# Optimization experiments

Measured on AMD Instinct MI355X. Metric: run time of the kernel, lower is better.

The kernel has to match this reference:

```python
import jax, jax.numpy as jnp
import numpy as np

EPS = 1e-5
QB = 127.0  # int8 activation quantization bound

def rmsnorm(x):
    # SimpleRMSNorm: x / rms(x), no learned scale
    return x * jax.lax.rsqrt(jnp.mean(x * x, axis=-1, keepdims=True) + EPS)

def activation_quant(x):
    # per-token absmax int8 quant-dequant
    scale = QB / jnp.clip(jnp.max(jnp.abs(x), axis=-1, keepdims=True), EPS)
    return jnp.clip(jnp.round(x * scale), -QB - 1, QB) / scale

def weight_quant(w):
    # per-tensor ternary quant-dequant (BitNet b1.58)
    scale = 1.0 / jnp.clip(jnp.mean(jnp.abs(w)), EPS)
    return jnp.clip(jnp.round(w * scale), -1.0, 1.0) / scale

def ste(x, q):
    # straight-through estimator: forward uses q, gradient flows to x
    return x + jax.lax.stop_gradient(q - x)

def bitlinear(x, w, b):
    xn = rmsnorm(x)
    xq = ste(xn, activation_quant(xn))
    wq = ste(w, weight_quant(w))
    # x: [b, s, d_in], w: [d_out, d_in] -> [b, s, d_out]
    return jnp.einsum('bsd,od->bso', xq, wq) + b

def setup_inputs() -> dict:
    key = jax.random.key(0)
    k1, k2, k3, k4, k5 = jax.random.split(key, 5)
    dim, inner = 1024, 4096
    x = jax.random.normal(k1, (4, 4096, dim), dtype=jnp.float32)
    w1 = jax.random.normal(k2, (inner, dim), dtype=jnp.float32) * (dim ** -0.5)
    b1 = jax.random.normal(k3, (inner,), dtype=jnp.float32) * 0.02
    w2 = jax.random.normal(k4, (dim, inner), dtype=jnp.float32) * (inner ** -0.5)
    b2 = jax.random.normal(k5, (dim,), dtype=jnp.float32) * 0.02
    return {"x": x, "w1": w1, "b1": b1, "w2": w2, "b2": b2}

def reference(x, w1, b1, w2, b2):
    h = jax.nn.gelu(bitlinear(x, w1, b1), approximate=False)  # torch nn.GELU default = exact erf
    # dropout p=0.0 is identity; post_act_ln disabled
    return bitlinear(h, w2, b2)
```

## Files before the change

### kernel.cpp

```cpp
#include <hip/hip_runtime.h>

#define TOK   16384
#define DIM   1024
#define INNER 4096
#define EPSF  1e-5f

typedef int v4i  __attribute__((ext_vector_type(4)));
typedef int v16i __attribute__((ext_vector_type(16)));

static __device__ __forceinline__ void async_copy16(const char* g, char* l) {
    __builtin_amdgcn_global_load_lds(
        (const __attribute__((address_space(1))) unsigned int*)g,
        (__attribute__((address_space(3))) unsigned int*)l, 16, 0, 0);
}

static __device__ __forceinline__ float bf2f(unsigned short u) {
    return __uint_as_float(((unsigned)u) << 16);
}
static __device__ __forceinline__ unsigned short f2bf(float f) {
    unsigned u = __float_as_uint(f);
    return (unsigned short)((u + 0x7fffu + ((u >> 16) & 1u)) >> 16);
}

static __device__ __forceinline__ float fast_erf(float z) {
    float az = fabsf(z);
    float tt = __builtin_amdgcn_rcpf(1.f + 0.3275911f * az);
    float poly = ((((1.061405429f * tt - 1.453152027f) * tt + 1.421413741f) * tt
                   - 0.284496736f) * tt + 0.254829592f) * tt;
    float er = 1.f - poly * __expf(-az * az);
    return copysignf(er, z);
}
static __device__ __forceinline__ float gelu_exact(float v) {
    return 0.5f * v * (1.f + fast_erf(v * 0.70710678118654752f));
}

static __device__ __forceinline__ float waveSum(float v) {
#pragma unroll
    for (int o = 32; o > 0; o >>= 1) v += __shfl_down(v, o, 64);
    return v;
}
static __device__ __forceinline__ float waveMax(float v) {
#pragma unroll
    for (int o = 32; o > 0; o >>= 1) v = fmaxf(v, __shfl_down(v, o, 64));
    return v;
}

__global__ void absmean_k(const float* __restrict__ w, int n4, float* __restrict__ acc) {
    int idx = blockIdx.x * blockDim.x + threadIdx.x;
    int stride = gridDim.x * blockDim.x;
    const float4* w4 = (const float4*)w;
    float s = 0.f;
    for (int i = idx; i < n4; i += stride) {
        float4 v = w4[i];
        s += fabsf(v.x) + fabsf(v.y) + fabsf(v.z) + fabsf(v.w);
    }
    __shared__ float sp[4];
    int wv = threadIdx.x >> 6, lane = threadIdx.x & 63;
    s = waveSum(s);
    if (lane == 0) sp[wv] = s;
    __syncthreads();
    if (threadIdx.x == 0) atomicAdd(acc, sp[0] + sp[1] + sp[2] + sp[3]);
}

__global__ void wquant_k(const float* __restrict__ w, int n,
                         const float* __restrict__ acc, float* __restrict__ wscale,
                         char* __restrict__ wq) {
    float mean = *acc / (float)n;
    float cl = fmaxf(mean, EPSF);
    float s = 1.f / cl;
    if (blockIdx.x == 0 && threadIdx.x == 0) *wscale = cl;
    int idx = blockIdx.x * blockDim.x + threadIdx.x;
    int stride = gridDim.x * blockDim.x;
    int n4 = n >> 2;
    const float4* w4 = (const float4*)w;
    unsigned* q4 = (unsigned*)wq;
    for (int i = idx; i < n4; i += stride) {
        float4 v = w4[i];
        float e[4] = {v.x, v.y, v.z, v.w};
        unsigned packed = 0;
#pragma unroll
        for (int j = 0; j < 4; j++) {
            float r = rintf(e[j] * s);
            r = fminf(fmaxf(r, -1.f), 1.f);
            packed |= ((unsigned)((int)r & 0xff)) << (8 * j);
        }
        q4[i] = packed;
    }
}

template <int D, int VPT>
__global__ void actquant_f32_k(const float* __restrict__ X, char* __restrict__ Q,
                               float* __restrict__ rs_out) {
    int token = blockIdx.x;
    int t = threadIdx.x;
    const float4* xp = (const float4*)(X + (long)token * D);
    float vals[VPT];
    float ss = 0.f, am = 0.f;
#pragma unroll
    for (int j = 0; j < VPT / 4; j++) {
        float4 v = xp[t * (VPT / 4) + j];
        vals[4 * j] = v.x; vals[4 * j + 1] = v.y; vals[4 * j + 2] = v.z; vals[4 * j + 3] = v.w;
        ss += v.x * v.x + v.y * v.y + v.z * v.z + v.w * v.w;
        am = fmaxf(am, fmaxf(fmaxf(fabsf(v.x), fabsf(v.y)), fmaxf(fabsf(v.z), fabsf(v.w))));
    }
    __shared__ float sp[8];
    __shared__ float bc[2];
    int wv = t >> 6, lane = t & 63;
    float S = waveSum(ss);
    float M = waveMax(am);
    if (lane == 0) { sp[wv] = S; sp[4 + wv] = M; }
    __syncthreads();
    if (t == 0) {
        float Sa = sp[0] + sp[1] + sp[2] + sp[3];
        float Ma = fmaxf(fmaxf(sp[4], sp[5]), fmaxf(sp[6], sp[7]));
        float rinv = rsqrtf(Sa * (1.f / (float)D) + EPSF);
        float amn = Ma * rinv;
        float scale = 127.f / fmaxf(amn, EPSF);
        rs_out[token] = 1.f / scale;
        bc[0] = rinv; bc[1] = scale;
    }
    __syncthreads();
    float rinv = bc[0], scale = bc[1];
    unsigned outw[VPT / 4];
#pragma unroll
    for (int j = 0; j < VPT; j++) {
        float r = rintf((vals[j] * rinv) * scale);
        r = fminf(fmaxf(r, -128.f), 127.f);
        unsigned qi = (unsigned)((int)r & 0xff) << (8 * (j & 3));
        if ((j & 3) == 0) outw[j / 4] = qi; else outw[j / 4] |= qi;
    }
    unsigned* qp = (unsigned*)(Q + (long)token * D);
#pragma unroll
    for (int j = 0; j < VPT / 4; j++) qp[t * (VPT / 4) + j] = outw[j];
}

template <int D, int VPT>
__global__ void actquant_bf16_k(const unsigned short* __restrict__ X, char* __restrict__ Q,
                                float* __restrict__ rs_out) {
    int token = blockIdx.x;
    int t = threadIdx.x;
    const uint4* xp = (const uint4*)(X + (long)token * D);
    float vals[VPT];
    float ss = 0.f, am = 0.f;
#pragma unroll
    for (int j = 0; j < VPT / 8; j++) {
        uint4 v = xp[t * (VPT / 8) + j];
        unsigned ws[4] = {v.x, v.y, v.z, v.w};
#pragma unroll
        for (int p = 0; p < 4; p++) {
            float f0 = gelu_exact(bf2f((unsigned short)(ws[p] & 0xffff)));
            float f1 = gelu_exact(bf2f((unsigned short)(ws[p] >> 16)));
            vals[8 * j + 2 * p] = f0; vals[8 * j + 2 * p + 1] = f1;
            ss += f0 * f0 + f1 * f1;
            am = fmaxf(am, fmaxf(fabsf(f0), fabsf(f1)));
        }
    }
    __shared__ float sp[8];
    __shared__ float bc[2];
    int wv = t >> 6, lane = t & 63;
    float S = waveSum(ss);
    float M = waveMax(am);
    if (lane == 0) { sp[wv] = S; sp[4 + wv] = M; }
    __syncthreads();
    if (t == 0) {
        float Sa = sp[0] + sp[1] + sp[2] + sp[3];
        float Ma = fmaxf(fmaxf(sp[4], sp[5]), fmaxf(sp[6], sp[7]));
        float rinv = rsqrtf(Sa * (1.f / (float)D) + EPSF);
        float amn = Ma * rinv;
        float scale = 127.f / fmaxf(amn, EPSF);
        rs_out[token] = 1.f / scale;
        bc[0] = rinv; bc[1] = scale;
    }
    __syncthreads();
    float rinv = bc[0], scale = bc[1];
    unsigned outw[4];
#pragma unroll
    for (int j = 0; j < VPT; j++) {
        float r = rintf((vals[j] * rinv) * scale);
        r = fminf(fmaxf(r, -128.f), 127.f);
        unsigned qi = (unsigned)((int)r & 0xff) << (8 * (j & 3));
        if ((j & 3) == 0) outw[j / 4] = qi; else outw[j / 4] |= qi;
    }
    uint4* qp = (uint4*)(Q + (long)token * D);
    qp[t] = make_uint4(outw[0], outw[1], outw[2], outw[3]);
}

template <int OUT_F32>
__global__ __launch_bounds__(512, 2) void gemm8_k(
    const char* __restrict__ A, const char* __restrict__ Bw,
    const float* __restrict__ rs, const float* __restrict__ wscale_p,
    const float* __restrict__ bias, void* __restrict__ outp,
    int M, int N, int K) {
    __shared__ char L[131072];
    int t = threadIdx.x;
    int lane = t & 63, wv = t >> 6;
    int l31 = lane & 31, kh = lane >> 5;
    int wmi = wv >> 2, wni = wv & 3;
    int m0 = blockIdx.y * 256, n0 = blockIdx.x * 256;

    int srow = t >> 3;
    int scol = ((t & 7) ^ (srow & 7)) * 16;
    const char* srcA = A + (long)(m0 + srow) * K + scol;
    const char* srcB = Bw + (long)(n0 + srow) * K + scol;
    char* ldsA = L + (size_t)t * 16;
    char* ldsB = L + 65536 + (size_t)t * 16;
    long k64 = (long)64 * K;

    auto stA = [&](int Tt, int half) {
        const char* g = srcA + (long)(half * 128) * K + (long)Tt * 128;
        char* l = ldsA + (Tt & 1) * 32768 + half * 16384;
        async_copy16(g, l);
        async_copy16(g + k64, l + 8192);
    };
    auto stB = [&](int Tt, int half) {
        const char* g = srcB + (long)(half * 128) * K + (long)Tt * 128;
        char* l = ldsB + (Tt & 1) * 32768 + half * 16384;
        async_copy16(g, l);
        async_copy16(g + k64, l + 8192);
    };

    int slot[4];
#pragma unroll
    for (int ks = 0; ks < 4; ks++) slot[ks] = ((2 * ks + kh) ^ (l31 & 7)) * 16;
    int rowA[2][2], rowB[2];
#pragma unroll
    for (int ih = 0; ih < 2; ih++)
#pragma unroll
        for (int il = 0; il < 2; il++)
            rowA[ih][il] = (ih * 128 + il * 64 + wmi * 32 + l31) * 128;
#pragma unroll
    for (int jh = 0; jh < 2; jh++) rowB[jh] = 65536 + (jh * 128 + wni * 32 + l31) * 128;

    v16i acc[4][2] = {};
    int nK = K >> 7;

    stA(0, 0); stA(0, 1); stB(0, 0); stB(0, 1);
    stB(1, 0); stA(1, 1);
    asm volatile("s_waitcnt vmcnt(4)" ::: "memory");
    asm volatile("s_barrier" ::: "memory");

#pragma unroll 2
    for (int T = 0; T < nK; ++T) {
        int bo = (T & 1) * 32768;
        v4i a[2][4], bb[4];
#pragma unroll
        for (int il = 0; il < 2; il++)
#pragma unroll
            for (int ks = 0; ks < 4; ks++)
                a[il][ks] = *(const v4i*)(L + bo + rowA[0][il] + slot[ks]);
#pragma unroll
        for (int ks = 0; ks < 4; ks++)
            bb[ks] = *(const v4i*)(L + bo + rowB[0] + slot[ks]);
        if (T + 1 < nK) stA(T + 1, 0);
        asm volatile("s_barrier" ::: "memory");
        __builtin_amdgcn_s_setprio(1);
#pragma unroll
        for (int ks = 0; ks < 4; ks++) {
            acc[0][0] = __builtin_amdgcn_mfma_i32_32x32x32_i8(a[0][ks], bb[ks], acc[0][0], 0, 0, 0);
            acc[1][0] = __builtin_amdgcn_mfma_i32_32x32x32_i8(a[1][ks], bb[ks], acc[1][0], 0, 0, 0);
        }
        __builtin_amdgcn_s_setprio(0);
        asm volatile("s_barrier" ::: "memory");
#pragma unroll
        for (int il = 0; il < 2; il++)
#pragma unroll
            for (int ks = 0; ks < 4; ks++)
                a[il][ks] = *(const v4i*)(L + bo + rowA[1][il] + slot[ks]);
        if (T + 1 < nK) stB(T + 1, 1);
        asm volatile("s_barrier" ::: "memory");
        __builtin_amdgcn_s_setprio(1);
#pragma unroll
        for (int ks = 0; ks < 4; ks++) {
            acc[2][0] = __builtin_amdgcn_mfma_i32_32x32x32_i8(a[0][ks], bb[ks], acc[2][0], 0, 0, 0);
            acc[3][0] = __builtin_amdgcn_mfma_i32_32x32x32_i8(a[1][ks], bb[ks], acc[3][0], 0, 0, 0);
        }
        __builtin_amdgcn_s_setprio(0);
        asm volatile("s_barrier" ::: "memory");
#pragma unroll
        for (int ks = 0; ks < 4; ks++)
            bb[ks] = *(const v4i*)(L + bo + rowB[1] + slot[ks]);
        if (T + 2 < nK) stB(T + 2, 0);
        asm volatile("s_barrier" ::: "memory");
        __builtin_amdgcn_s_setprio(1);
#pragma unroll
        for (int ks = 0; ks < 4; ks++) {
            acc[2][1] = __builtin_amdgcn_mfma_i32_32x32x32_i8(a[0][ks], bb[ks], acc[2][1], 0, 0, 0);
            acc[3][1] = __builtin_amdgcn_mfma_i32_32x32x32_i8(a[1][ks], bb[ks], acc[3][1], 0, 0, 0);
        }
        __builtin_amdgcn_s_setprio(0);
        asm volatile("s_barrier" ::: "memory");
#pragma unroll
        for (int il = 0; il < 2; il++)
#pragma unroll
            for (int ks = 0; ks < 4; ks++)
                a[il][ks] = *(const v4i*)(L + bo + rowA[0][il] + slot[ks]);
        if (T + 2 < nK) stA(T + 2, 1);
        asm volatile("s_barrier" ::: "memory");
        __builtin_amdgcn_s_setprio(1);
#pragma unroll
        for (int ks = 0; ks < 4; ks++) {
            acc[0][1] = __builtin_amdgcn_mfma_i32_32x32x32_i8(a[0][ks], bb[ks], acc[0][1], 0, 0, 0);
            acc[1][1] = __builtin_amdgcn_mfma_i32_32x32x32_i8(a[1][ks], bb[ks], acc[1][1], 0, 0, 0);
        }
        __builtin_amdgcn_s_setprio(0);
        asm volatile("s_waitcnt vmcnt(4)" ::: "memory");
        asm volatile("s_barrier" ::: "memory");
    }

    float wsc = *wscale_p;
    float bv[2];
#pragma unroll
    for (int j = 0; j < 2; j++) bv[j] = bias[n0 + j * 128 + wni * 32 + l31];
#pragma unroll
    for (int i = 0; i < 4; i++) {
        int mbase = m0 + i * 64 + wmi * 32 + 4 * kh;
        float fsv[16];
#pragma unroll
        for (int rg = 0; rg < 16; rg++)
            fsv[rg] = rs[mbase + (rg & 3) + 8 * (rg >> 2)] * wsc;
#pragma unroll
        for (int j = 0; j < 2; j++) {
            int ng = n0 + j * 128 + wni * 32 + l31;
#pragma unroll
            for (int rg = 0; rg < 16; rg++) {
                int mg = mbase + (rg & 3) + 8 * (rg >> 2);
                float v = (float)acc[i][j][rg] * fsv[rg] + bv[j];
                long idx = (long)mg * N + ng;
                if (OUT_F32) ((float*)outp)[idx] = v;
                else ((unsigned short*)outp)[idx] = f2bf(v);
            }
        }
    }
}

extern "C" void kernel_launch(void* const* d_in, const int* in_sizes, int n_in,
                              void* d_out, int out_size, void* d_ws, size_t ws_size,
                              hipStream_t stream) {
    const float* x  = (const float*)d_in[0];
    const float* w1 = (const float*)d_in[1];
    const float* b1 = (const float*)d_in[2];
    const float* w2 = (const float*)d_in[3];
    const float* b2 = (const float*)d_in[4];
    float* out = (float*)d_out;

    char* ws = (char*)d_ws;
    float* acc1 = (float*)(ws + 0);
    float* acc2 = (float*)(ws + 4);
    float* wsc1 = (float*)(ws + 8);
    float* wsc2 = (float*)(ws + 12);
    size_t off = 256;
    char* w1q = ws + off; off += (size_t)INNER * DIM;
    char* w2q = ws + off; off += (size_t)INNER * DIM;
    char* xq1 = ws + off; off += (size_t)TOK * DIM;
    float* rs1 = (float*)(ws + off); off += (size_t)TOK * 4;
    char* xq2 = ws + off; off += (size_t)TOK * INNER;
    float* rs2 = (float*)(ws + off); off += (size_t)TOK * 4;
    unsigned short* h = (unsigned short*)(ws + off);

    hipMemsetAsync(d_ws, 0, 16, stream);

    int nw = INNER * DIM;
    absmean_k<<<1024, 256, 0, stream>>>(w1, nw / 4, acc1);
    absmean_k<<<1024, 256, 0, stream>>>(w2, nw / 4, acc2);
    wquant_k<<<2048, 256, 0, stream>>>(w1, nw, acc1, wsc1, w1q);
    wquant_k<<<2048, 256, 0, stream>>>(w2, nw, acc2, wsc2, w2q);

    actquant_f32_k<DIM, 4><<<TOK, 256, 0, stream>>>(x, xq1, rs1);
    gemm8_k<0><<<dim3(INNER / 256, TOK / 256), 512, 0, stream>>>(
        xq1, w1q, rs1, wsc1, b1, (void*)h, TOK, INNER, DIM);
    actquant_bf16_k<INNER, 16><<<TOK, 256, 0, stream>>>(h, xq2, rs2);
    gemm8_k<1><<<dim3(DIM / 256, TOK / 256), 512, 0, stream>>>(
        xq2, w2q, rs2, wsc2, b2, (void*)out, TOK, DIM, INNER);
}
```

Baseline: 391.4 us.

## Restructure int8 GEMM LDS layout to k-major slabs with per-kstep pipelining

Replaces the row-major XOR-swizzled LDS tile layout with a k-block-major layout where each 16-byte k-chunk of all 256 rows is stored contiguously, and reassigns warps to contiguous 128x64 output subtiles. The main loop now issues one k-step of 8 MFMAs per barrier pair, interleaving the four async stage-loads for the next tile across k-steps with a single-tile lookahead instead of the previous two-stage staggered schedule. This aims for conflict-free LDS reads without swizzle and better MFMA density per barrier, at the cost of losing deeper prefetch and changing global load coalescing, since each thread now reads 16 bytes per row at stride K.

Result: slower. 439.2 us (+12.2%).

```diff
diff --git a/kernel.cpp b/kernel.cpp
--- a/kernel.cpp
+++ b/kernel.cpp
@@ -198,129 +198,87 @@
     int wmi = wv >> 2, wni = wv & 3;
     int m0 = blockIdx.y * 256, n0 = blockIdx.x * 256;
 
-    int srow = t >> 3;
-    int scol = ((t & 7) ^ (srow & 7)) * 16;
-    const char* srcA = A + (long)(m0 + srow) * K + scol;
-    const char* srcB = Bw + (long)(n0 + srow) * K + scol;
-    char* ldsA = L + (size_t)t * 16;
-    char* ldsB = L + 65536 + (size_t)t * 16;
-    long k64 = (long)64 * K;
-
-    auto stA = [&](int Tt, int half) {
-        const char* g = srcA + (long)(half * 128) * K + (long)Tt * 128;
-        char* l = ldsA + (Tt & 1) * 32768 + half * 16384;
+    const char* srcA0 = A  + (long)(m0 + (t & 255)) * K + ((t >> 8) * 16);
+    const char* srcB0 = Bw + (long)(n0 + (t & 255)) * K + ((t >> 8) * 16);
+    char* dA = L + (size_t)t * 16;
+    char* dB = L + 32768 + (size_t)t * 16;
+
+    auto stA = [&](int Tt, int kb) {
+        const char* g = srcA0 + ((long)Tt << 7) + kb * 64;
+        char* l = dA + (Tt & 1) * 65536 + kb * 16384;
         async_copy16(g, l);
-        async_copy16(g + k64, l + 8192);
+        async_copy16(g + 32, l + 8192);
     };
-    auto stB = [&](int Tt, int half) {
-        const char* g = srcB + (long)(half * 128) * K + (long)Tt * 128;
-        char* l = ldsB + (Tt & 1) * 32768 + half * 16384;
+    auto stB = [&](int Tt, int kb) {
+        const char* g = srcB0 + ((long)Tt << 7) + kb * 64;
+        char* l = dB + (Tt & 1) * 65536 + kb * 16384;
         async_copy16(g, l);
-        async_copy16(g + k64, l + 8192);
+        async_copy16(g + 32, l + 8192);
     };
 
-    int slot[4];
-#pragma unroll
-    for (int ks = 0; ks < 4; ks++) slot[ks] = ((2 * ks + kh) ^ (l31 & 7)) * 16;
-    int rowA[2][2], rowB[2];
-#pragma unroll
-    for (int ih = 0; ih < 2; ih++)
-#pragma unroll
-        for (int il = 0; il < 2; il++)
-            rowA[ih][il] = (ih * 128 + il * 64 + wmi * 32 + l31) * 128;
-#pragma unroll
-    for (int jh = 0; jh < 2; jh++) rowB[jh] = 65536 + (jh * 128 + wni * 32 + l31) * 128;
+    const char* rdA = L + kh * 4096 + (size_t)(wmi * 128 + l31) * 16;
+    const char* rdB = L + 32768 + kh * 4096 + (size_t)(wni * 64 + l31) * 16;
 
     v16i acc[4][2] = {};
     int nK = K >> 7;
 
-    stA(0, 0); stA(0, 1); stB(0, 0); stB(0, 1);
-    stB(1, 0); stA(1, 1);
+    stA(0, 0); stB(0, 0); stA(0, 1); stB(0, 1);
     asm volatile("s_waitcnt vmcnt(4)" ::: "memory");
-    asm volatile("s_barrier" ::: "memory");
-
-#pragma unroll 2
+    __builtin_amdgcn_s_barrier();
+
     for (int T = 0; T < nK; ++T) {
-        int bo = (T & 1) * 32768;
-        v4i a[2][4], bb[4];
-#pragma unroll
-        for (int il = 0; il < 2; il++)
-#pragma unroll
-            for (int ks = 0; ks < 4; ks++)
-                a[il][ks] = *(const v4i*)(L + bo + rowA[0][il] + slot[ks]);
-#pragma unroll
-        for (int ks = 0; ks < 4; ks++)
-            bb[ks] = *(const v4i*)(L + bo + rowB[0] + slot[ks]);
-        if (T + 1 < nK) stA(T + 1, 0);
-        asm volatile("s_barrier" ::: "memory");
-        __builtin_amdgcn_s_setprio(1);
-#pragma unroll
-        for (int ks = 0; ks < 4; ks++) {
-            acc[0][0] = __builtin_amdgcn_mfma_i32_32x32x32_i8(a[0][ks], bb[ks], acc[0][0], 0, 0, 0);
-            acc[1][0] = __builtin_amdgcn_mfma_i32_32x32x32_i8(a[1][ks], bb[ks], acc[1][0], 0, 0, 0);
+        int bo = (T & 1) * 65536;
+        bool pre = (T + 1 < nK);
+#pragma unroll
+        for (int ks = 0; ks < 4; ++ks) {
+            const char* pa = rdA + bo + ks * 8192;
+            const char* pb = rdB + bo + ks * 8192;
+            v4i a0 = *(const v4i*)(pa);
+            v4i a1 = *(const v4i*)(pa + 512);
+            v4i a2 = *(const v4i*)(pa + 1024);
+            v4i a3 = *(const v4i*)(pa + 1536);
+            v4i b0 = *(const v4i*)(pb);
+            v4i b1 = *(const v4i*)(pb + 512);
+            if (pre) {
+                if (ks == 0) stA(T + 1, 0);
+                else if (ks == 1) stB(T + 1, 0);
+                else if (ks == 2) stA(T + 1, 1);
+                else stB(T + 1, 1);
+            }
+            __builtin_amdgcn_s_barrier();
+            __builtin_amdgcn_s_setprio(1);
+            acc[0][0] = __builtin_amdgcn_mfma_i32_32x32x32_i8(a0, b0, acc[0][0], 0, 0, 0);
+            acc[0][1] = __builtin_amdgcn_mfma_i32_32x32x32_i8(a0, b1, acc[0][1], 0, 0, 0);
+            acc[1][0] = __builtin_amdgcn_mfma_i32_32x32x32_i8(a1, b0, acc[1][0], 0, 0, 0);
+            acc[1][1] = __builtin_amdgcn_mfma_i32_32x32x32_i8(a1, b1, acc[1][1], 0, 0, 0);
+            acc[2][0] = __builtin_amdgcn_mfma_i32_32x32x32_i8(a2, b0, acc[2][0], 0, 0, 0);
+            acc[2][1] = __builtin_amdgcn_mfma_i32_32x32x32_i8(a2, b1, acc[2][1], 0, 0, 0);
+            acc[3][0] = __builtin_amdgcn_mfma_i32_32x32x32_i8(a3, b0, acc[3][0], 0, 0, 0);
+            acc[3][1] = __builtin_amdgcn_mfma_i32_32x32x32_i8(a3, b1, acc[3][1], 0, 0, 0);
+            __builtin_amdgcn_s_setprio(0);
+            if (ks == 1) {
+                if (pre) asm volatile("s_waitcnt vmcnt(4)" ::: "memory");
+                else     asm volatile("s_waitcnt vmcnt(0)" ::: "memory");
+            }
+            if (ks == 3 && pre) asm volatile("s_waitcnt vmcnt(4)" ::: "memory");
+            __builtin_amdgcn_s_barrier();
         }
-        __builtin_amdgcn_s_setprio(0);
-        asm volatile("s_barrier" ::: "memory");
-#pragma unroll
-        for (int il = 0; il < 2; il++)
-#pragma unroll
-            for (int ks = 0; ks < 4; ks++)
-                a[il][ks] = *(const v4i*)(L + bo + rowA[1][il] + slot[ks]);
-        if (T + 1 < nK) stB(T + 1, 1);
-        asm volatile("s_barrier" ::: "memory");
-        __builtin_amdgcn_s_setprio(1);
-#pragma unroll
-        for (int ks = 0; ks < 4; ks++) {
-            acc[2][0] = __builtin_amdgcn_mfma_i32_32x32x32_i8(a[0][ks], bb[ks], acc[2][0], 0, 0, 0);
-            acc[3][0] = __builtin_amdgcn_mfma_i32_32x32x32_i8(a[1][ks], bb[ks], acc[3][0], 0, 0, 0);
-        }
-        __builtin_amdgcn_s_setprio(0);
-        asm volatile("s_barrier" ::: "memory");
-#pragma unroll
-        for (int ks = 0; ks < 4; ks++)
-            bb[ks] = *(const v4i*)(L + bo + rowB[1] + slot[ks]);
-        if (T + 2 < nK) stB(T + 2, 0);
-        asm volatile("s_barrier" ::: "memory");
-        __builtin_amdgcn_s_setprio(1);
-#pragma unroll
-        for (int ks = 0; ks < 4; ks++) {
-            acc[2][1] = __builtin_amdgcn_mfma_i32_32x32x32_i8(a[0][ks], bb[ks], acc[2][1], 0, 0, 0);
-            acc[3][1] = __builtin_amdgcn_mfma_i32_32x32x32_i8(a[1][ks], bb[ks], acc[3][1], 0, 0, 0);
-        }
-        __builtin_amdgcn_s_setprio(0);
-        asm volatile("s_barrier" ::: "memory");
-#pragma unroll
-        for (int il = 0; il < 2; il++)
-#pragma unroll
-            for (int ks = 0; ks < 4; ks++)
-                a[il][ks] = *(const v4i*)(L + bo + rowA[0][il] + slot[ks]);
-        if (T + 2 < nK) stA(T + 2, 1);
-        asm volatile("s_barrier" ::: "memory");
-        __builtin_amdgcn_s_setprio(1);
-#pragma unroll
-        for (int ks = 0; ks < 4; ks++) {
-            acc[0][1] = __builtin_amdgcn_mfma_i32_32x32x32_i8(a[0][ks], bb[ks], acc[0][1], 0, 0, 0);
-            acc[1][1] = __builtin_amdgcn_mfma_i32_32x32x32_i8(a[1][ks], bb[ks], acc[1][1], 0, 0, 0);
-        }
-        __builtin_amdgcn_s_setprio(0);
-        asm volatile("s_waitcnt vmcnt(4)" ::: "memory");
-        asm volatile("s_barrier" ::: "memory");
     }
 
     float wsc = *wscale_p;
     float bv[2];
 #pragma unroll
-    for (int j = 0; j < 2; j++) bv[j] = bias[n0 + j * 128 + wni * 32 + l31];
+    for (int j = 0; j < 2; j++) bv[j] = bias[n0 + wni * 64 + j * 32 + l31];
 #pragma unroll
     for (int i = 0; i < 4; i++) {
-        int mbase = m0 + i * 64 + wmi * 32 + 4 * kh;
+        int mbase = m0 + wmi * 128 + i * 32 + 4 * kh;
         float fsv[16];
 #pragma unroll
         for (int rg = 0; rg < 16; rg++)
             fsv[rg] = rs[mbase + (rg & 3) + 8 * (rg >> 2)] * wsc;
 #pragma unroll
         for (int j = 0; j < 2; j++) {
-            int ng = n0 + j * 128 + wni * 32 + l31;
+            int ng = n0 + wni * 64 + j * 32 + l31;
 #pragma unroll
             for (int rg = 0; rg < 16; rg++) {
                 int mg = mbase + (rg & 3) + 8 * (rg >> 2);
```

## Rework int8 GEMM LDS layout, swizzle block order, and keep fragments in registers

Applied to the files above, without the earlier changes.

Changes the LDS tile layout from XOR-swizzled rows to a 16-row by 16-byte subtile layout that matches the MFMA fragment reads. Adds an XCD-aware block-index swizzle so neighbouring tiles share L2, and keeps both A halves and both B halves in separate registers so fragments are not reloaded within a K step. The aim is fewer LDS bank conflicts and redundant LDS reads, plus better cache locality. In exchange it uses more VGPRs under the 2-waves-per-SIMD launch bound, and the final iteration now drains with vmcnt(0).

New measurement: 390.4 us. About the same (-0.3%).

```diff
diff --git a/kernel.cpp b/kernel.cpp
--- a/kernel.cpp
+++ b/kernel.cpp
@@ -186,7 +186,7 @@
 }
 
 template <int OUT_F32>
-__global__ __launch_bounds__(512, 2) void gemm8_k(
+__global__ __launch_bounds__(512, 2) void gemm8r_k(
     const char* __restrict__ A, const char* __restrict__ Bw,
     const float* __restrict__ rs, const float* __restrict__ wscale_p,
     const float* __restrict__ bias, void* __restrict__ outp,
@@ -196,40 +196,46 @@
     int lane = t & 63, wv = t >> 6;
     int l31 = lane & 31, kh = lane >> 5;
     int wmi = wv >> 2, wni = wv & 3;
-    int m0 = blockIdx.y * 256, n0 = blockIdx.x * 256;
-
-    int srow = t >> 3;
-    int scol = ((t & 7) ^ (srow & 7)) * 16;
-    const char* srcA = A + (long)(m0 + srow) * K + scol;
-    const char* srcB = Bw + (long)(n0 + srow) * K + scol;
-    char* ldsA = L + (size_t)t * 16;
-    char* ldsB = L + 65536 + (size_t)t * 16;
-    long k64 = (long)64 * K;
-
-    auto stA = [&](int Tt, int half) {
-        const char* g = srcA + (long)(half * 128) * K + (long)Tt * 128;
-        char* l = ldsA + (Tt & 1) * 32768 + half * 16384;
-        async_copy16(g, l);
-        async_copy16(g + k64, l + 8192);
+
+    int gx = gridDim.x;
+    int nwg = gx * gridDim.y;
+    int bid = blockIdx.y * gx + blockIdx.x;
+    int swz = (bid & 7) * (nwg >> 3) + (bid >> 3);
+    int bx = swz % gx, by = swz / gx;
+    int m0 = by * 256, n0 = bx * 256;
+
+    int sl = lane & 15;
+    const char* srcA = A  + (long)(m0 + wv * 16 + sl) * K + ((lane >> 4) * 16);
+    const char* srcB = Bw + (long)(n0 + wv * 16 + sl) * K + ((lane >> 4) * 16);
+    char* dA = L + wv * 1024 + lane * 16;
+    char* dB = L + 65536 + wv * 1024 + lane * 16;
+
+    auto stA = [&](int Tt, int ih) {
+        const char* g = srcA + (long)ih * 128 * K + ((long)Tt << 7);
+        char* d = dA + (Tt & 1) * 32768 + ih * 16384;
+        async_copy16(g, d);
+        async_copy16(g + 64, d + 8192);
     };
-    auto stB = [&](int Tt, int half) {
-        const char* g = srcB + (long)(half * 128) * K + (long)Tt * 128;
-        char* l = ldsB + (Tt & 1) * 32768 + half * 16384;
-        async_copy16(g, l);
-        async_copy16(g + k64, l + 8192);
+    auto stB = [&](int Tt, int jh) {
+        const char* g = srcB + (long)jh * 128 * K + ((long)Tt << 7);
+        char* d = dB + (Tt & 1) * 32768 + jh * 16384;
+        async_copy16(g, d);
+        async_copy16(g + 64, d + 8192);
     };
 
-    int slot[4];
-#pragma unroll
-    for (int ks = 0; ks < 4; ks++) slot[ks] = ((2 * ks + kh) ^ (l31 & 7)) * 16;
-    int rowA[2][2], rowB[2];
-#pragma unroll
-    for (int ih = 0; ih < 2; ih++)
-#pragma unroll
-        for (int il = 0; il < 2; il++)
-            rowA[ih][il] = (ih * 128 + il * 64 + wmi * 32 + l31) * 128;
-#pragma unroll
-    for (int jh = 0; jh < 2; jh++) rowB[jh] = 65536 + (jh * 128 + wni * 32 + l31) * 128;
+    int tOff[4];
+#pragma unroll
+    for (int ks = 0; ks < 4; ks++) {
+        int tt = 2 * ks + kh;
+        tOff[ks] = (tt >> 2) * 8192 + (tt & 3) * 256;
+    }
+    int rA[2], rB;
+#pragma unroll
+    for (int il = 0; il < 2; il++) {
+        int r = il * 64 + wmi * 32 + l31;
+        rA[il] = (r >> 4) * 1024 + (r & 15) * 16;
+    }
+    { int r = wni * 32 + l31; rB = (r >> 4) * 1024 + (r & 15) * 16; }
 
     v16i acc[4][2] = {};
     int nK = K >> 7;
@@ -239,71 +245,69 @@
     asm volatile("s_waitcnt vmcnt(4)" ::: "memory");
     asm volatile("s_barrier" ::: "memory");
 
-#pragma unroll 2
     for (int T = 0; T < nK; ++T) {
         int bo = (T & 1) * 32768;
-        v4i a[2][4], bb[4];
-#pragma unroll
-        for (int il = 0; il < 2; il++)
-#pragma unroll
-            for (int ks = 0; ks < 4; ks++)
-                a[il][ks] = *(const v4i*)(L + bo + rowA[0][il] + slot[ks]);
+        bool pre1 = (T + 1 < nK), pre2 = (T + 2 < nK);
+        const char* pA0 = L + bo;
+        const char* pA1 = L + bo + 16384;
+        const char* pB0 = L + 65536 + bo;
+        const char* pB1 = L + 65536 + bo + 16384;
+        v4i a0[2][4], a1[2][4], b0[4], b1[4];
+#pragma unroll
+        for (int ks = 0; ks < 4; ks++) {
+            a0[0][ks] = *(const v4i*)(pA0 + tOff[ks] + rA[0]);
+            a0[1][ks] = *(const v4i*)(pA0 + tOff[ks] + rA[1]);
+            b0[ks]    = *(const v4i*)(pB0 + tOff[ks] + rB);
+        }
+        if (pre1) stA(T + 1, 0);
+        asm volatile("s_barrier" ::: "memory");
+        __builtin_amdgcn_s_setprio(1);
+#pragma unroll
+        for (int ks = 0; ks < 4; ks++) {
+            acc[0][0] = __builtin_amdgcn_mfma_i32_32x32x32_i8(a0[0][ks], b0[ks], acc[0][0], 0, 0, 0);
+            acc[1][0] = __builtin_amdgcn_mfma_i32_32x32x32_i8(a0[1][ks], b0[ks], acc[1][0], 0, 0, 0);
+        }
+        __builtin_amdgcn_s_setprio(0);
+        asm volatile("s_barrier" ::: "memory");
+#pragma unroll
+        for (int ks = 0; ks < 4; ks++) {
+            a1[0][ks] = *(const v4i*)(pA1 + tOff[ks] + rA[0]);
+            a1[1][ks] = *(const v4i*)(pA1 + tOff[ks] + rA[1]);
+        }
+        if (pre1) stB(T + 1, 1);
+        asm volatile("s_barrier" ::: "memory");
+        __builtin_amdgcn_s_setprio(1);
+#pragma unroll
+        for (int ks = 0; ks < 4; ks++) {
+            acc[2][0] = __builtin_amdgcn_mfma_i32_32x32x32_i8(a1[0][ks], b0[ks], acc[2][0], 0, 0, 0);
+            acc[3][0] = __builtin_amdgcn_mfma_i32_32x32x32_i8(a1[1][ks], b0[ks], acc[3][0], 0, 0, 0);
+        }
+        __builtin_amdgcn_s_setprio(0);
+        asm volatile("s_barrier" ::: "memory");
 #pragma unroll
         for (int ks = 0; ks < 4; ks++)
-            bb[ks] = *(const v4i*)(L + bo + rowB[0] + slot[ks]);
-        if (T + 1 < nK) stA(T + 1, 0);
+            b1[ks] = *(const v4i*)(pB1 + tOff[ks] + rB);
+        if (pre2) stB(T + 2, 0);
         asm volatile("s_barrier" ::: "memory");
         __builtin_amdgcn_s_setprio(1);
 #pragma unroll
         for (int ks = 0; ks < 4; ks++) {
-            acc[0][0] = __builtin_amdgcn_mfma_i32_32x32x32_i8(a[0][ks], bb[ks], acc[0][0], 0, 0, 0);
-            acc[1][0] = __builtin_amdgcn_mfma_i32_32x32x32_i8(a[1][ks], bb[ks], acc[1][0], 0, 0, 0);
+            acc[2][1] = __builtin_amdgcn_mfma_i32_32x32x32_i8(a1[0][ks], b1[ks], acc[2][1], 0, 0, 0);
+            acc[3][1] = __builtin_amdgcn_mfma_i32_32x32x32_i8(a1[1][ks], b1[ks], acc[3][1], 0, 0, 0);
         }
         __builtin_amdgcn_s_setprio(0);
         asm volatile("s_barrier" ::: "memory");
-#pragma unroll
-        for (int il = 0; il < 2; il++)
-#pragma unroll
-            for (int ks = 0; ks < 4; ks++)
-                a[il][ks] = *(const v4i*)(L + bo + rowA[1][il] + slot[ks]);
-        if (T + 1 < nK) stB(T + 1, 1);
+        if (pre2) stA(T + 2, 1);
         asm volatile("s_barrier" ::: "memory");
         __builtin_amdgcn_s_setprio(1);
 #pragma unroll
         for (int ks = 0; ks < 4; ks++) {
-            acc[2][0] = __builtin_amdgcn_mfma_i32_32x32x32_i8(a[0][ks], bb[ks], acc[2][0], 0, 0, 0);
-            acc[3][0] = __builtin_amdgcn_mfma_i32_32x32x32_i8(a[1][ks], bb[ks], acc[3][0], 0, 0, 0);
+            acc[0][1] = __builtin_amdgcn_mfma_i32_32x32x32_i8(a0[0][ks], b1[ks], acc[0][1], 0, 0, 0);
+            acc[1][1] = __builtin_amdgcn_mfma_i32_32x32x32_i8(a0[1][ks], b1[ks], acc[1][1], 0, 0, 0);
         }
         __builtin_amdgcn_s_setprio(0);
-        asm volatile("s_barrier" ::: "memory");
-#pragma unroll
-        for (int ks = 0; ks < 4; ks++)
-            bb[ks] = *(const v4i*)(L + bo + rowB[1] + slot[ks]);
-        if (T + 2 < nK) stB(T + 2, 0);
-        asm volatile("s_barrier" ::: "memory");
-        __builtin_amdgcn_s_setprio(1);
-#pragma unroll
-        for (int ks = 0; ks < 4; ks++) {
-            acc[2][1] = __builtin_amdgcn_mfma_i32_32x32x32_i8(a[0][ks], bb[ks], acc[2][1], 0, 0, 0);
-            acc[3][1] = __builtin_amdgcn_mfma_i32_32x32x32_i8(a[1][ks], bb[ks], acc[3][1], 0, 0, 0);
-        }
-        __builtin_amdgcn_s_setprio(0);
-        asm volatile("s_barrier" ::: "memory");
-#pragma unroll
-        for (int il = 0; il < 2; il++)
-#pragma unroll
-            for (int ks = 0; ks < 4; ks++)
-                a[il][ks] = *(const v4i*)(L + bo + rowA[0][il] + slot[ks]);
-        if (T + 2 < nK) stA(T + 2, 1);
-        asm volatile("s_barrier" ::: "memory");
-        __builtin_amdgcn_s_setprio(1);
-#pragma unroll
-        for (int ks = 0; ks < 4; ks++) {
-            acc[0][1] = __builtin_amdgcn_mfma_i32_32x32x32_i8(a[0][ks], bb[ks], acc[0][1], 0, 0, 0);
-            acc[1][1] = __builtin_amdgcn_mfma_i32_32x32x32_i8(a[1][ks], bb[ks], acc[1][1], 0, 0, 0);
-        }
-        __builtin_amdgcn_s_setprio(0);
-        asm volatile("s_waitcnt vmcnt(4)" ::: "memory");
+        if (pre2) asm volatile("s_waitcnt vmcnt(4)" ::: "memory");
+        else      asm volatile("s_waitcnt vmcnt(0)" ::: "memory");
         asm volatile("s_barrier" ::: "memory");
     }
 
@@ -366,9 +370,9 @@
     wquant_k<<<2048, 256, 0, stream>>>(w2, nw, acc2, wsc2, w2q);
 
     actquant_f32_k<DIM, 4><<<TOK, 256, 0, stream>>>(x, xq1, rs1);
-    gemm8_k<0><<<dim3(INNER / 256, TOK / 256), 512, 0, stream>>>(
+    gemm8r_k<0><<<dim3(INNER / 256, TOK / 256), 512, 0, stream>>>(
         xq1, w1q, rs1, wsc1, b1, (void*)h, TOK, INNER, DIM);
     actquant_bf16_k<INNER, 16><<<TOK, 256, 0, stream>>>(h, xq2, rs2);
-    gemm8_k<1><<<dim3(DIM / 256, TOK / 256), 512, 0, stream>>>(
+    gemm8r_k<1><<<dim3(DIM / 256, TOK / 256), 512, 0, stream>>>(
         xq2, w2q, rs2, wsc2, b2, (void*)out, TOK, DIM, INNER);
 }
```
